# Performance work log

Measured on AMD Instinct MI355X. Metric: run time of the kernel, lower is better.

The kernel has to match this reference:

```python
import jax, jax.numpy as jnp
import numpy as np

D = 1024      # hidden_dim
H = 16        # num_heads
KV = 8        # num_kv_heads
HD = D // H   # head_size = 64
M = 3584      # intermediate_dim
E = 8         # num_local_experts
TOPK = 2      # num_experts_per_tok
EPS = 1e-6
ROPE_THETA = 10000.0


def setup_inputs() -> dict:
    key = jax.random.key(0)
    ks = jax.random.split(key, 12)
    s = 0.02
    B, S = 2, 1024
    return {
        "x": jax.random.normal(ks[0], (B, S, D), jnp.float32),
        "ln1_w": jnp.ones((D,), jnp.float32),
        "ln2_w": jnp.ones((D,), jnp.float32),
        "wq": jax.random.normal(ks[1], (D, H * HD), jnp.float32) * s,
        "wk": jax.random.normal(ks[2], (D, KV * HD), jnp.float32) * s,
        "wv": jax.random.normal(ks[3], (D, KV * HD), jnp.float32) * s,
        "wo": jax.random.normal(ks[4], (H * HD, D), jnp.float32) * s,
        "router_w": jax.random.normal(ks[5], (D, E), jnp.float32) * s,
        "w_gate": jax.random.normal(ks[6], (E, D, M), jnp.float32) * s,
        "w_up": jax.random.normal(ks[7], (E, D, M), jnp.float32) * s,
        "w_down": jax.random.normal(ks[8], (E, M, D), jnp.float32) * s,
    }


def _rmsnorm(x, w, eps=EPS):
    xf = x.astype(jnp.float32)
    var = jnp.mean(xf * xf, axis=-1, keepdims=True)
    return (xf * jax.lax.rsqrt(var + eps)).astype(x.dtype) * w


def _rope(q, k):
    # q: [B,S,H,HD], k: [B,S,KV,HD]
    S = q.shape[1]
    inv_freq = 1.0 / (ROPE_THETA ** (jnp.arange(0, HD, 2, dtype=jnp.float32) / HD))
    ang = jnp.arange(S, dtype=jnp.float32)[:, None] * inv_freq[None, :]  # [S, HD/2]
    cos = jnp.concatenate([jnp.cos(ang), jnp.cos(ang)], axis=-1)[None, :, None, :]
    sin = jnp.concatenate([jnp.sin(ang), jnp.sin(ang)], axis=-1)[None, :, None, :]

    def rot_half(t):
        t1, t2 = jnp.split(t, 2, axis=-1)
        return jnp.concatenate([-t2, t1], axis=-1)

    return q * cos + rot_half(q) * sin, k * cos + rot_half(k) * sin


def reference(x, ln1_w, ln2_w, wq, wk, wv, wo, router_w, w_gate, w_up, w_down):
    B, S, _ = x.shape

    # ---- self-attention block ----
    h = _rmsnorm(x, ln1_w)
    q = (h @ wq).reshape(B, S, H, HD)
    k = (h @ wk).reshape(B, S, KV, HD)
    v = (h @ wv).reshape(B, S, KV, HD)
    q, k = _rope(q, k)
    rep = H // KV
    k = jnp.repeat(k, rep, axis=2)  # [B,S,H,HD]
    v = jnp.repeat(v, rep, axis=2)
    scores = jnp.einsum("bqhd,bkhd->bhqk", q, k) / jnp.sqrt(jnp.float32(HD))
    causal = jnp.tril(jnp.ones((S, S), bool))
    scores = jnp.where(causal[None, None], scores, jnp.finfo(scores.dtype).min)
    attn = jax.nn.softmax(scores, axis=-1)
    ao = jnp.einsum("bhqk,bkhd->bqhd", attn, v).reshape(B, S, H * HD)
    x = x + ao @ wo

    # ---- sparse MoE block (top-2 routing, SwiGLU experts) ----
    h = _rmsnorm(x, ln2_w)
    logits = h @ router_w                       # [B,S,E]
    probs = jax.nn.softmax(logits, axis=-1)
    topv, topi = jax.lax.top_k(probs, TOPK)     # [B,S,K]
    topv = topv / jnp.sum(topv, axis=-1, keepdims=True)
    # dense combine weights [B,S,E]: zero for unselected experts
    weights = jnp.sum(jax.nn.one_hot(topi, E, dtype=h.dtype) * topv[..., None], axis=-2)
    gate = jnp.einsum("bsd,edm->bsem", h, w_gate)
    up = jnp.einsum("bsd,edm->bsem", h, w_up)
    act = jax.nn.silu(gate) * up * weights[..., None]
    moe = jnp.einsum("bsem,emd->bsd", act, w_down)
    return x + moe
```

## Files before the change

### kernel.cpp

```cpp
#include <hip/hip_runtime.h>

typedef __attribute__((ext_vector_type(8))) short short8;
typedef __attribute__((ext_vector_type(4))) float f32x4;
typedef unsigned int u32;

#define DI static __device__ __forceinline__

DI unsigned short f2bf(float f) {
  unsigned u = __builtin_bit_cast(unsigned, f);
  u += 0x7fffu + ((u >> 16) & 1u);
  return (unsigned short)(u >> 16);
}
DI float bf2f(unsigned short b) {
  unsigned u = ((unsigned)b) << 16;
  return __builtin_bit_cast(float, u);
}

DI void gload16(const unsigned short* g, unsigned short* l) {
  __builtin_amdgcn_global_load_lds(
      (const __attribute__((address_space(1))) u32*)g,
      (__attribute__((address_space(3))) u32*)l, 16, 0, 0);
}

static constexpr int NT   = 2048;
static constexpr int SEQ  = 1024;
static constexpr int DIM  = 1024;
static constexpr int NH   = 16;
static constexpr int NKV  = 8;
static constexpr int HD   = 64;
static constexpr int MDIM = 3584;
static constexpr int NE   = 8;
static constexpr int QW   = 2048;
static constexpr int GUW  = 2 * MDIM;

template <int ROWMAP>
__global__ void __launch_bounds__(256) transpose_kernel(
    const float* __restrict__ in, unsigned short* __restrict__ out,
    int R, int C, size_t in_estride, size_t out_estride) {
  __shared__ unsigned short tl[64][66];
  int e = blockIdx.z;
  const float* ip = in + (size_t)e * in_estride;
  unsigned short* op = out + (size_t)e * out_estride;
  int c0 = blockIdx.x * 64, r0 = blockIdx.y * 64;
  int tid = threadIdx.x;
  {
    int lr = tid >> 4, lc = (tid & 15) * 4;
#pragma unroll
    for (int p = 0; p < 4; ++p) {
      int r = p * 16 + lr;
      float4 v = *(const float4*)(ip + (size_t)(r0 + r) * C + c0 + lc);
      tl[lc + 0][r] = f2bf(v.x);
      tl[lc + 1][r] = f2bf(v.y);
      tl[lc + 2][r] = f2bf(v.z);
      tl[lc + 3][r] = f2bf(v.w);
    }
  }
  __syncthreads();
  {
    int c = tid >> 2, rc = (tid & 3) * 16;
    unsigned short tmp[16];
#pragma unroll
    for (int j = 0; j < 8; ++j) {
      u32 w = *(const u32*)&tl[c][rc + j * 2];
      tmp[j * 2] = (unsigned short)w;
      tmp[j * 2 + 1] = (unsigned short)(w >> 16);
    }
    int cg = c0 + c;
    int orow;
    if (ROWMAP == 0) orow = cg;
    else orow = ((cg >> 4) << 5) + (cg & 15) + (ROWMAP == 2 ? 16 : 0);
    unsigned short* dst = op + (size_t)orow * R + r0 + rc;
#pragma unroll
    for (int j = 0; j < 2; ++j)
      *(uint4*)(dst + j * 8) = *(const uint4*)&tmp[j * 8];
  }
}

__global__ void __launch_bounds__(256) vtrans_kernel(const unsigned short* __restrict__ qkv,
                                                     unsigned short* __restrict__ vT) {
  __shared__ unsigned short tl[64][66];
  int s0 = blockIdx.x * 64;
  int kvh = blockIdx.y;
  int b = blockIdx.z;
  int tid = threadIdx.x;
  {
    int r = tid >> 2, cc = (tid & 3) * 16;
    const unsigned short* src =
        qkv + ((size_t)(b * SEQ + s0 + r)) * QW + (DIM + NKV * HD + kvh * HD) + cc;
    unsigned short tmp[16];
    *(uint4*)&tmp[0] = *(const uint4*)src;
    *(uint4*)&tmp[8] = *(const uint4*)(src + 8);
#pragma unroll
    for (int j = 0; j < 16; ++j) tl[cc + j][r] = tmp[j];
  }
  __syncthreads();
  {
    int h = tid >> 2, sc = (tid & 3) * 16;
    unsigned short o[16];
#pragma unroll
    for (int j = 0; j < 16; ++j) o[j] = tl[h][sc + j];
    unsigned short* dst = vT + (((size_t)(b * NKV + kvh) * HD + h) * SEQ) + s0 + sc;
    *(uint4*)dst = *(const uint4*)&o[0];
    *(uint4*)(dst + 8) = *(const uint4*)&o[8];
  }
}

__global__ void __launch_bounds__(256) rmsnorm_kernel(const float* __restrict__ x,
                                                      const float* __restrict__ w,
                                                      unsigned short* __restrict__ out) {
  int row = blockIdx.x;
  const float* xr = x + (size_t)row * DIM;
  int i = threadIdx.x * 4;
  float4 v = *(const float4*)(xr + i);
  float s = v.x * v.x + v.y * v.y + v.z * v.z + v.w * v.w;
  for (int o = 32; o; o >>= 1) s += __shfl_xor(s, o);
  __shared__ float red[4];
  if ((threadIdx.x & 63) == 0) red[threadIdx.x >> 6] = s;
  __syncthreads();
  s = red[0] + red[1] + red[2] + red[3];
  float r = rsqrtf(s * (1.0f / DIM) + 1e-6f);
  float4 wv = *(const float4*)(w + i);
  ushort4 o4;
  o4.x = f2bf(v.x * r * wv.x);
  o4.y = f2bf(v.y * r * wv.y);
  o4.z = f2bf(v.z * r * wv.z);
  o4.w = f2bf(v.w * r * wv.w);
  *(ushort4*)(out + (size_t)row * DIM + i) = o4;
}

template <int GATHER, int EPI, int NNT>
__global__ void __launch_bounds__(256) gemmT_kernel(
    const unsigned short* __restrict__ A, int lda,
    const unsigned short* __restrict__ B, int ldb, size_t b_estride,
    void* __restrict__ Cv, int ldc,
    const float* __restrict__ resid,
    int M, int K,
    const int* __restrict__ lists, const int* __restrict__ cnt,
    int ks_count, size_t ks_stride) {
  constexpr int BN = NNT * 32;
  constexpr int NBLK = BN / 64;
  int zz = blockIdx.z;
  int e = zz / ks_count, ks = zz - e * ks_count;
  int KL = K / ks_count;
  int kbase = ks * KL;

  int count = M;
  const int* lst = nullptr;
  if (GATHER != 0) {
    count = cnt[e];
    if (count <= 0) return;
    lst = lists + e * NT;
    B += b_estride * (size_t)e;
  }
  int m0 = blockIdx.y * 128;
  if (m0 >= count) return;
  int n0 = blockIdx.x * BN;

  __shared__ unsigned short sB[3][BN * 32];

  int tid = threadIdx.x, w = tid >> 6, lane = tid & 63;
  int l15 = lane & 15, lhi = lane >> 4;
  int wm = w >> 1, wn = w & 1;

  int srow = w * 16 + (lane >> 2);
  int schunk = (((lane & 3) - ((lane >> 3) & 3)) & 3) * 8;
  const unsigned short* bSrc[NBLK];
#pragma unroll
  for (int s = 0; s < NBLK; ++s)
    bSrc[s] = B + (size_t)(n0 + s * 64 + srow) * ldb + kbase + schunk;
  unsigned ldst = (unsigned)(w * 16) * 32;

  auto stage = [&](int buf, int k0) {
#pragma unroll
    for (int s = 0; s < NBLK; ++s)
      gload16(bSrc[s] + k0, &sB[buf][ldst + s * 64 * 32]);
  };

  const unsigned short* aFrag[4];
#pragma unroll
  for (int mi = 0; mi < 4; ++mi) {
    int mr = m0 + wm * 64 + mi * 16 + l15;
    if (mr > count - 1) mr = count - 1;
    int ar;
    if (GATHER == 0) ar = mr;
    else {
      int pid = lst[mr];
      ar = (GATHER == 1) ? (pid >> 1) : pid;
    }
    aFrag[mi] = A + (size_t)ar * lda + kbase + lhi * 8;
  }

  f32x4 acc[4][NNT] = {};
  int fslot = ((lhi + (l15 >> 1)) & 3) * 8;
  int boff[NNT];
#pragma unroll
  for (int t = 0; t < NNT; ++t) {
    int col = wn * (BN / 2) + t * 16 + l15;
    boff[t] = col * 32 + fslot;
  }

  int nsteps = KL / 32;
  stage(0, 0);
  if (nsteps > 1) stage(1, 32);

  int cur = 0, stg = 2;
  for (int t = 0; t < nsteps; ++t) {
    if (t + 1 < nsteps) {
      if constexpr (NBLK == 1) asm volatile("s_waitcnt vmcnt(1)" ::: "memory");
      else                     asm volatile("s_waitcnt vmcnt(2)" ::: "memory");
    } else {
      asm volatile("s_waitcnt vmcnt(0)" ::: "memory");
    }
    __builtin_amdgcn_s_barrier();
    __builtin_amdgcn_sched_barrier(0);
    short8 af[4];
#pragma unroll
    for (int mi = 0; mi < 4; ++mi)
      af[mi] = *(const short8*)(aFrag[mi] + t * 32);
    if (t + 2 < nsteps) stage(stg, (t + 2) * 32);
    const unsigned short* pb = sB[cur];
    short8 bfr[NNT];
#pragma unroll
    for (int q = 0; q < NNT; ++q) bfr[q] = *(const short8*)&pb[boff[q]];
    __builtin_amdgcn_s_setprio(1);
#pragma unroll
    for (int mi = 0; mi < 4; ++mi)
#pragma unroll
      for (int ni = 0; ni < NNT; ++ni)
        acc[mi][ni] =
            __builtin_amdgcn_mfma_f32_16x16x32_bf16(af[mi], bfr[ni], acc[mi][ni], 0, 0, 0);
    __builtin_amdgcn_s_setprio(0);
    cur = (cur == 2) ? 0 : cur + 1;
    stg = (stg == 2) ? 0 : stg + 1;
  }

#pragma unroll
  for (int mi = 0; mi < 4; ++mi) {
#pragma unroll
    for (int r = 0; r < 4; ++r) {
      int mr = m0 + wm * 64 + mi * 16 + lhi * 4 + r;
      if (GATHER != 0 && mr >= count) continue;
      size_t crow = (GATHER != 0) ? (size_t)lst[mr] : (size_t)mr;
      if (EPI == 3) {
        float wgt = resid[crow];
        int colbase = (n0 + wn * (BN / 2)) >> 1;
#pragma unroll
        for (int ni = 0; ni < NNT; ni += 2) {
          float g = acc[mi][ni][r], u = acc[mi][ni + 1][r];
          float sv = g / (1.f + __expf(-g));
          ((unsigned short*)Cv)[crow * ldc + colbase + (ni >> 1) * 16 + l15] =
              f2bf(sv * u * wgt);
        }
      } else {
#pragma unroll
        for (int ni = 0; ni < NNT; ++ni) {
          int n = n0 + wn * (BN / 2) + ni * 16 + l15;
          float val = acc[mi][ni][r];
          if (EPI == 0)
            ((unsigned short*)Cv)[crow * ldc + n] = f2bf(val);
          else if (EPI == 1)
            ((float*)Cv)[crow * ldc + n] = val + resid[crow * ldc + n];
          else
            ((float*)Cv)[(size_t)ks * ks_stride + crow * ldc + n] = val;
        }
      }
    }
  }
}

__global__ void __launch_bounds__(256) rope_kernel(unsigned short* __restrict__ qkv) {
  int g = blockIdx.x * 256 + threadIdx.x;
  int i = g & 31;
  int hh = (g >> 5) % (NH + NKV);
  int tok = g / (32 * (NH + NKV));
  if (tok >= NT) return;
  int s = tok & (SEQ - 1);
  float inv = exp2f((float)i * (-13.287712379549449f / 32.0f));
  float ang = (float)s * inv;
  float sn = sinf(ang);
  float c = cosf(ang);
  int col = (hh < NH) ? hh * HD : DIM + (hh - NH) * HD;
  unsigned short* ptr = qkv + (size_t)tok * QW + col;
  float a = bf2f(ptr[i]), b2 = bf2f(ptr[i + 32]);
  ptr[i] = f2bf(a * c - b2 * sn);
  ptr[i + 32] = f2bf(b2 * c + a * sn);
}

__global__ void __launch_bounds__(64) attn_kernel(const unsigned short* __restrict__ qkv,
                                                  const unsigned short* __restrict__ vT,
                                                  unsigned short* __restrict__ ao) {
  __shared__ unsigned short Ps[16 * 64];
  int bid = blockIdx.x;
  int qt = bid & 63;
  int h = (bid >> 6) & 15;
  int b = bid >> 10;
  int lane = threadIdx.x, l15 = lane & 15, lhi = lane >> 4;
  int q0 = qt * 16, kvh = h >> 1;
  int kcol = DIM + kvh * HD;

  const unsigned short* qp = qkv + ((size_t)(b * SEQ + q0 + l15)) * QW + h * HD + lhi * 8;
  short8 aq0 = *(const short8*)qp;
  short8 aq1 = *(const short8*)(qp + 32);

  const unsigned short* vbase = vT + ((size_t)(b * NKV + kvh) * HD) * SEQ;

  float m[4] = {-1e30f, -1e30f, -1e30f, -1e30f};
  float l[4] = {0.f, 0.f, 0.f, 0.f};
  f32x4 accO[4] = {};

  int nkb = (qt >> 2) + 1;
  for (int kb_ = 0; kb_ < nkb; ++kb_) {
    int kbase = kb_ * 64;
    f32x4 s[4];
#pragma unroll
    for (int ct = 0; ct < 4; ++ct) {
      const unsigned short* kp =
          qkv + ((size_t)(b * SEQ + kbase + ct * 16 + l15)) * QW + kcol + lhi * 8;
      short8 k0v = *(const short8*)kp;
      short8 k1v = *(const short8*)(kp + 32);
      f32x4 a = {};
      a = __builtin_amdgcn_mfma_f32_16x16x32_bf16(aq0, k0v, a, 0, 0, 0);
      a = __builtin_amdgcn_mfma_f32_16x16x32_bf16(aq1, k1v, a, 0, 0, 0);
      int kpos = kbase + ct * 16 + l15;
#pragma unroll
      for (int r = 0; r < 4; ++r) {
        float v = a[r] * 0.125f;
        if (kpos > q0 + lhi * 4 + r) v = -1e30f;
        s[ct][r] = v;
      }
    }
    float nm[4], al[4], rs[4];
#pragma unroll
    for (int r = 0; r < 4; ++r) {
      float mb = fmaxf(fmaxf(s[0][r], s[1][r]), fmaxf(s[2][r], s[3][r]));
      mb = fmaxf(mb, __shfl_xor(mb, 1));
      mb = fmaxf(mb, __shfl_xor(mb, 2));
      mb = fmaxf(mb, __shfl_xor(mb, 4));
      mb = fmaxf(mb, __shfl_xor(mb, 8));
      nm[r] = fmaxf(m[r], mb);
      al[r] = __expf(m[r] - nm[r]);
      m[r] = nm[r];
      rs[r] = 0.f;
    }
#pragma unroll
    for (int ct = 0; ct < 4; ++ct) {
#pragma unroll
      for (int r = 0; r < 4; ++r) {
        float p = __expf(s[ct][r] - nm[r]);
        rs[r] += p;
        int q = lhi * 4 + r;
        Ps[q * 64 + ((ct * 16 + l15) ^ (lhi << 4))] = f2bf(p);
      }
    }
#pragma unroll
    for (int r = 0; r < 4; ++r) {
      rs[r] += __shfl_xor(rs[r], 1);
      rs[r] += __shfl_xor(rs[r], 2);
      rs[r] += __shfl_xor(rs[r], 4);
      rs[r] += __shfl_xor(rs[r], 8);
      l[r] = l[r] * al[r] + rs[r];
    }
#pragma unroll
    for (int dt = 0; dt < 4; ++dt)
#pragma unroll
      for (int r = 0; r < 4; ++r) accO[dt][r] *= al[r];

    int pswz = (l15 >> 2) << 4;
    short8 ap0 = *(const short8*)&Ps[l15 * 64 + ((lhi * 8) ^ pswz)];
    short8 ap1 = *(const short8*)&Ps[l15 * 64 + ((32 + lhi * 8) ^ pswz)];
#pragma unroll
    for (int dt = 0; dt < 4; ++dt) {
#pragma unroll
      for (int ks = 0; ks < 2; ++ks) {
        const unsigned short* vp =
            vbase + ((size_t)(dt * 16 + l15)) * SEQ + kbase + ks * 32 + lhi * 8;
        short8 vf = *(const short8*)vp;
        accO[dt] = __builtin_amdgcn_mfma_f32_16x16x32_bf16(ks ? ap1 : ap0, vf, accO[dt], 0, 0, 0);
      }
    }
  }
  float invl[4];
#pragma unroll
  for (int r = 0; r < 4; ++r) invl[r] = 1.f / l[r];
#pragma unroll
  for (int dt = 0; dt < 4; ++dt)
#pragma unroll
    for (int r = 0; r < 4; ++r)
      ao[((size_t)(b * SEQ + q0 + lhi * 4 + r)) * DIM + h * HD + dt * 16 + l15] =
          f2bf(accO[dt][r] * invl[r]);
}

__global__ void zero_cnt_kernel(int* __restrict__ cnt) {
  if (threadIdx.x < NE) cnt[threadIdx.x] = 0;
}

__global__ void __launch_bounds__(64) router_kernel(const float* __restrict__ x2,
                                                    const float* __restrict__ ln2w,
                                                    const float* __restrict__ rw,
                                                    float* __restrict__ wts,
                                                    int* __restrict__ cnt,
                                                    int* __restrict__ lists) {
  int t = blockIdx.x, lane = threadIdx.x;
  const float* xr = x2 + (size_t)t * DIM;
  float xs[16];
  double ssq = 0.0;
#pragma unroll
  for (int j = 0; j < 16; ++j) {
    xs[j] = xr[lane + j * 64];
    ssq += (double)xs[j] * xs[j];
  }
  for (int o = 32; o; o >>= 1) ssq += __shfl_xor(ssq, o);
  double r = rsqrt(ssq * (1.0 / DIM) + 1e-6);
  double p[NE] = {};
#pragma unroll
  for (int j = 0; j < 16; ++j) {
    int i = lane + j * 64;
    double hv = (double)xs[j] * r * (double)ln2w[i];
    const float* rwp = rw + (size_t)i * NE;
#pragma unroll
    for (int e = 0; e < NE; ++e) p[e] += hv * (double)rwp[e];
  }
  for (int o = 32; o; o >>= 1) {
#pragma unroll
    for (int e = 0; e < NE; ++e) p[e] += __shfl_xor(p[e], o);
  }
  if (lane == 0) {
    int i1 = 0;
    for (int e = 1; e < NE; ++e)
      if (p[e] > p[i1]) i1 = e;
    int i2 = (i1 == 0) ? 1 : 0;
    for (int e = 0; e < NE; ++e)
      if (e != i1 && p[e] > p[i2]) i2 = e;
    double mx = fmax(p[i1], p[i2]);
    double e1 = exp(p[i1] - mx), e2 = exp(p[i2] - mx);
    double inv = 1.0 / (e1 + e2);
    wts[t * 2] = (float)(e1 * inv);
    wts[t * 2 + 1] = (float)(e2 * inv);
    int pos1 = atomicAdd(&cnt[i1], 1);
    lists[i1 * NT + pos1] = t * 2;
    int pos2 = atomicAdd(&cnt[i2], 1);
    lists[i2 * NT + pos2] = t * 2 + 1;
  }
}

__global__ void __launch_bounds__(256) combine_kernel(const float* __restrict__ x2,
                                                      const float* __restrict__ part,
                                                      float* __restrict__ out) {
  const size_t KSS = (size_t)2 * NT * DIM;
  size_t idx = ((size_t)blockIdx.x * 256 + threadIdx.x) * 4;
  size_t t = idx >> 10;
  size_t d = idx & 1023;
  float4 o = *(const float4*)(x2 + idx);
#pragma unroll
  for (int s = 0; s < 4; ++s) {
    float4 b0 = *(const float4*)(part + s * KSS + (t * 2) * DIM + d);
    float4 c0 = *(const float4*)(part + s * KSS + (t * 2 + 1) * DIM + d);
    o.x += b0.x + c0.x;
    o.y += b0.y + c0.y;
    o.z += b0.z + c0.z;
    o.w += b0.w + c0.w;
  }
  *(float4*)(out + idx) = o;
}

extern "C" void kernel_launch(void* const* d_in, const int* in_sizes, int n_in,
                              void* d_out, int out_size, void* d_ws, size_t ws_size,
                              hipStream_t stream) {
  const float* x   = (const float*)d_in[0];
  const float* ln1 = (const float*)d_in[1];
  const float* ln2 = (const float*)d_in[2];
  const float* wq  = (const float*)d_in[3];
  const float* wk  = (const float*)d_in[4];
  const float* wv  = (const float*)d_in[5];
  const float* wo  = (const float*)d_in[6];
  const float* rw  = (const float*)d_in[7];
  const float* wg  = (const float*)d_in[8];
  const float* wu  = (const float*)d_in[9];
  const float* wd  = (const float*)d_in[10];
  float* out = (float*)d_out;

  char* p = (char*)d_ws;
  auto take = [&](size_t bytes) {
    char* q = p;
    p += (bytes + 255) & ~(size_t)255;
    return q;
  };
  unsigned short* wguT = (unsigned short*)take((size_t)NE * GUW * DIM * 2);
  unsigned short* wdT  = (unsigned short*)take((size_t)NE * DIM * MDIM * 2);
  float*          x2   = (float*)take((size_t)NT * DIM * 4);
  unsigned short* h2   = (unsigned short*)take((size_t)NT * DIM * 2);
  float*          part = (float*)take((size_t)4 * 2 * NT * DIM * 4);
  unsigned short* act  = (unsigned short*)take((size_t)2 * NT * MDIM * 2);
  float*          wtsb = (float*)take((size_t)2 * NT * 4);
  int*            cntb = (int*)take(NE * 4);
  int*            listsb = (int*)take((size_t)NE * NT * 4);
  char* X = p;
  unsigned short* wqkvT = (unsigned short*)X;
  unsigned short* woT   = wqkvT + (size_t)QW * DIM;
  unsigned short* h1    = woT + (size_t)DIM * DIM;
  unsigned short* qkv   = h1 + (size_t)NT * DIM;
  unsigned short* aob   = qkv + (size_t)NT * QW;
  unsigned short* vT    = aob + (size_t)NT * DIM;

  transpose_kernel<0><<<dim3(16, 16, 1), 256, 0, stream>>>(wq, wqkvT, DIM, DIM, 0, 0);
  transpose_kernel<0><<<dim3(8, 16, 1), 256, 0, stream>>>(wk, wqkvT + (size_t)DIM * DIM, DIM, 512, 0, 0);
  transpose_kernel<0><<<dim3(8, 16, 1), 256, 0, stream>>>(wv, wqkvT + (size_t)(DIM + 512) * DIM, DIM, 512, 0, 0);
  transpose_kernel<0><<<dim3(16, 16, 1), 256, 0, stream>>>(wo, woT, DIM, DIM, 0, 0);
  transpose_kernel<1><<<dim3(56, 16, NE), 256, 0, stream>>>(
      wg, wguT, DIM, MDIM, (size_t)DIM * MDIM, (size_t)GUW * DIM);
  transpose_kernel<2><<<dim3(56, 16, NE), 256, 0, stream>>>(
      wu, wguT, DIM, MDIM, (size_t)DIM * MDIM, (size_t)GUW * DIM);
  transpose_kernel<0><<<dim3(16, 56, NE), 256, 0, stream>>>(
      wd, wdT, MDIM, DIM, (size_t)MDIM * DIM, (size_t)DIM * MDIM);

  rmsnorm_kernel<<<NT, 256, 0, stream>>>(x, ln1, h1);
  gemmT_kernel<0, 0, 2><<<dim3(QW / 64, NT / 128, 1), 256, 0, stream>>>(
      h1, DIM, wqkvT, DIM, 0, qkv, QW, nullptr, NT, DIM, nullptr, nullptr, 1, 0);
  rope_kernel<<<(NT * (NH + NKV) * 32) / 256, 256, 0, stream>>>(qkv);
  vtrans_kernel<<<dim3(SEQ / 64, NKV, 2), 256, 0, stream>>>(qkv, vT);
  attn_kernel<<<NT * NH / 16, 64, 0, stream>>>(qkv, vT, aob);
  gemmT_kernel<0, 1, 2><<<dim3(DIM / 64, NT / 128, 1), 256, 0, stream>>>(
      aob, DIM, woT, DIM, 0, x2, DIM, x, NT, DIM, nullptr, nullptr, 1, 0);

  rmsnorm_kernel<<<NT, 256, 0, stream>>>(x2, ln2, h2);
  zero_cnt_kernel<<<1, 64, 0, stream>>>(cntb);
  router_kernel<<<NT, 64, 0, stream>>>(x2, ln2, rw, wtsb, cntb, listsb);

  gemmT_kernel<1, 3, 4><<<dim3(GUW / 128, 16, NE), 256, 0, stream>>>(
      h2, DIM, wguT, DIM, (size_t)GUW * DIM, act, MDIM, wtsb, 0, DIM, listsb, cntb, 1, 0);
  gemmT_kernel<2, 2, 4><<<dim3(DIM / 128, 16, NE * 4), 256, 0, stream>>>(
      act, MDIM, wdT, MDIM, (size_t)DIM * MDIM, part, DIM, nullptr, 0, MDIM, listsb, cntb,
      4, (size_t)2 * NT * DIM);

  combine_kernel<<<(NT * DIM) / 1024, 256, 0, stream>>>(x2, part, out);
}
```

Measured before the change: 617.3 us.

## Prefetch A fragments one step ahead and unify GEMM tile width to 128

The GEMM kernel now loads the A-operand register fragments for step t+1 while computing step t, ping-ponging two register sets inside a loop unrolled by two, with vmcnt waits adjusted to cover the extra in-flight global loads. The template parameter for N tile width is removed and every GEMM uses BN=128, so the QKV and output-projection GEMMs get wider tiles and half as many blocks. This is meant to hide global-load latency on A, at the cost of more registers and fewer blocks for the dense GEMMs. The unrolled-by-two loop assumes an even step count, and the hand-written vmcnt counts must match the actual number of outstanding loads.

```diff
diff --git a/kernel.cpp b/kernel.cpp
--- a/kernel.cpp
+++ b/kernel.cpp
@@ -128,7 +128,7 @@
   *(ushort4*)(out + (size_t)row * DIM + i) = o4;
 }
 
-template <int GATHER, int EPI, int NNT>
+template <int GATHER, int EPI>
 __global__ void __launch_bounds__(256) gemmT_kernel(
     const unsigned short* __restrict__ A, int lda,
     const unsigned short* __restrict__ B, int ldb, size_t b_estride,
@@ -137,8 +137,8 @@
     int M, int K,
     const int* __restrict__ lists, const int* __restrict__ cnt,
     int ks_count, size_t ks_stride) {
-  constexpr int BN = NNT * 32;
-  constexpr int NBLK = BN / 64;
+  constexpr int BN = 128;
+  constexpr int NBLK = 2;
   int zz = blockIdx.z;
   int e = zz / ks_count, ks = zz - e * ks_count;
   int KL = K / ks_count;
@@ -190,48 +190,53 @@
     aFrag[mi] = A + (size_t)ar * lda + kbase + lhi * 8;
   }
 
-  f32x4 acc[4][NNT] = {};
+  f32x4 acc[4][4] = {};
   int fslot = ((lhi + (l15 >> 1)) & 3) * 8;
-  int boff[NNT];
-#pragma unroll
-  for (int t = 0; t < NNT; ++t) {
-    int col = wn * (BN / 2) + t * 16 + l15;
+  int boff[4];
+#pragma unroll
+  for (int t = 0; t < 4; ++t) {
+    int col = wn * 64 + t * 16 + l15;
     boff[t] = col * 32 + fslot;
   }
 
   int nsteps = KL / 32;
+  int cur = 0, stg = 2;
+
+  short8 afA[4], afB[4];
   stage(0, 0);
-  if (nsteps > 1) stage(1, 32);
-
-  int cur = 0, stg = 2;
-  for (int t = 0; t < nsteps; ++t) {
-    if (t + 1 < nsteps) {
-      if constexpr (NBLK == 1) asm volatile("s_waitcnt vmcnt(1)" ::: "memory");
-      else                     asm volatile("s_waitcnt vmcnt(2)" ::: "memory");
-    } else {
-      asm volatile("s_waitcnt vmcnt(0)" ::: "memory");
-    }
+  stage(1, 32);
+#pragma unroll
+  for (int mi = 0; mi < 4; ++mi) afA[mi] = *(const short8*)(aFrag[mi]);
+
+  auto body = [&](int T, short8(&C)[4], short8(&N)[4]) {
+    if (T + 1 < nsteps) asm volatile("s_waitcnt vmcnt(6)" ::: "memory");
+    else                asm volatile("s_waitcnt vmcnt(4)" ::: "memory");
     __builtin_amdgcn_s_barrier();
     __builtin_amdgcn_sched_barrier(0);
-    short8 af[4];
+    int tn = (T + 1 < nsteps) ? T + 1 : T;
 #pragma unroll
     for (int mi = 0; mi < 4; ++mi)
-      af[mi] = *(const short8*)(aFrag[mi] + t * 32);
-    if (t + 2 < nsteps) stage(stg, (t + 2) * 32);
+      N[mi] = *(const short8*)(aFrag[mi] + (size_t)tn * 32);
+    if (T + 2 < nsteps) stage(stg, (T + 2) * 32);
     const unsigned short* pb = sB[cur];
-    short8 bfr[NNT];
-#pragma unroll
-    for (int q = 0; q < NNT; ++q) bfr[q] = *(const short8*)&pb[boff[q]];
+    short8 bfr[4];
+#pragma unroll
+    for (int q = 0; q < 4; ++q) bfr[q] = *(const short8*)&pb[boff[q]];
     __builtin_amdgcn_s_setprio(1);
 #pragma unroll
     for (int mi = 0; mi < 4; ++mi)
 #pragma unroll
-      for (int ni = 0; ni < NNT; ++ni)
+      for (int ni = 0; ni < 4; ++ni)
         acc[mi][ni] =
-            __builtin_amdgcn_mfma_f32_16x16x32_bf16(af[mi], bfr[ni], acc[mi][ni], 0, 0, 0);
+            __builtin_amdgcn_mfma_f32_16x16x32_bf16(C[mi], bfr[ni], acc[mi][ni], 0, 0, 0);
     __builtin_amdgcn_s_setprio(0);
     cur = (cur == 2) ? 0 : cur + 1;
     stg = (stg == 2) ? 0 : stg + 1;
+  };
+
+  for (int t = 0; t < nsteps; t += 2) {
+    body(t, afA, afB);
+    body(t + 1, afB, afA);
   }
 
 #pragma unroll
@@ -243,9 +248,9 @@
       size_t crow = (GATHER != 0) ? (size_t)lst[mr] : (size_t)mr;
       if (EPI == 3) {
         float wgt = resid[crow];
-        int colbase = (n0 + wn * (BN / 2)) >> 1;
-#pragma unroll
-        for (int ni = 0; ni < NNT; ni += 2) {
+        int colbase = (n0 + wn * 64) >> 1;
+#pragma unroll
+        for (int ni = 0; ni < 4; ni += 2) {
           float g = acc[mi][ni][r], u = acc[mi][ni + 1][r];
           float sv = g / (1.f + __expf(-g));
           ((unsigned short*)Cv)[crow * ldc + colbase + (ni >> 1) * 16 + l15] =
@@ -253,8 +258,8 @@
         }
       } else {
 #pragma unroll
-        for (int ni = 0; ni < NNT; ++ni) {
-          int n = n0 + wn * (BN / 2) + ni * 16 + l15;
+        for (int ni = 0; ni < 4; ++ni) {
+          int n = n0 + wn * 64 + ni * 16 + l15;
           float val = acc[mi][ni][r];
           if (EPI == 0)
             ((unsigned short*)Cv)[crow * ldc + n] = f2bf(val);
@@ -514,21 +519,21 @@
       wd, wdT, MDIM, DIM, (size_t)MDIM * DIM, (size_t)DIM * MDIM);
 
   rmsnorm_kernel<<<NT, 256, 0, stream>>>(x, ln1, h1);
-  gemmT_kernel<0, 0, 2><<<dim3(QW / 64, NT / 128, 1), 256, 0, stream>>>(
+  gemmT_kernel<0, 0><<<dim3(QW / 128, NT / 128, 1), 256, 0, stream>>>(
       h1, DIM, wqkvT, DIM, 0, qkv, QW, nullptr, NT, DIM, nullptr, nullptr, 1, 0);
   rope_kernel<<<(NT * (NH + NKV) * 32) / 256, 256, 0, stream>>>(qkv);
   vtrans_kernel<<<dim3(SEQ / 64, NKV, 2), 256, 0, stream>>>(qkv, vT);
   attn_kernel<<<NT * NH / 16, 64, 0, stream>>>(qkv, vT, aob);
-  gemmT_kernel<0, 1, 2><<<dim3(DIM / 64, NT / 128, 1), 256, 0, stream>>>(
+  gemmT_kernel<0, 1><<<dim3(DIM / 128, NT / 128, 1), 256, 0, stream>>>(
       aob, DIM, woT, DIM, 0, x2, DIM, x, NT, DIM, nullptr, nullptr, 1, 0);
 
   rmsnorm_kernel<<<NT, 256, 0, stream>>>(x2, ln2, h2);
   zero_cnt_kernel<<<1, 64, 0, stream>>>(cntb);
   router_kernel<<<NT, 64, 0, stream>>>(x2, ln2, rw, wtsb, cntb, listsb);
 
-  gemmT_kernel<1, 3, 4><<<dim3(GUW / 128, 16, NE), 256, 0, stream>>>(
+  gemmT_kernel<1, 3><<<dim3(GUW / 128, 16, NE), 256, 0, stream>>>(
       h2, DIM, wguT, DIM, (size_t)GUW * DIM, act, MDIM, wtsb, 0, DIM, listsb, cntb, 1, 0);
-  gemmT_kernel<2, 2, 4><<<dim3(DIM / 128, 16, NE * 4), 256, 0, stream>>>(
+  gemmT_kernel<2, 2><<<dim3(DIM / 128, 16, NE * 4), 256, 0, stream>>>(
       act, MDIM, wdT, MDIM, (size_t)DIM * MDIM, part, DIM, nullptr, 0, MDIM, listsb, cntb,
       4, (size_t)2 * NT * DIM);
 
```

New measurement: 613.9 us. No clear change (-0.5%).
